# Kernel tuning notes

Hardware: AMD Instinct MI355X
Metric: run time of the kernel (lower is better)

Reference implementation:

```python
import jax, jax.numpy as jnp
import numpy as np

N = 500_000   # nodes
E = 1_250_000 # edges
CIN, H = 2, 64
EPS = 1e-5


def setup_inputs() -> dict:
    key = jax.random.key(0)
    ks = jax.random.split(key, 16)
    def w(k, i, o):
        return jax.random.normal(k, (i, o), jnp.float32) / np.sqrt(i)
    return {
        "x": jax.random.normal(ks[0], (N, CIN), jnp.float32),
        "edge_index": jax.random.randint(ks[1], (2, E), 0, N, jnp.int64),
        # SAGEConv layer 1 (lin_l on aggregated neighbors has bias, lin_r on root has none)
        "W1l": w(ks[2], CIN, H), "b1": jnp.zeros((H,), jnp.float32), "W1r": w(ks[3], CIN, H),
        "g1": jnp.ones((H,), jnp.float32), "be1": jnp.zeros((H,), jnp.float32),
        # SAGEConv layer 2
        "W2l": w(ks[4], H, H), "b2": jnp.zeros((H,), jnp.float32), "W2r": w(ks[5], H, H),
        "g2": jnp.ones((H,), jnp.float32), "be2": jnp.zeros((H,), jnp.float32),
        # SAGEConv layer 3 -> 1 channel
        "W3l": w(ks[6], H, 1), "b3": jnp.zeros((1,), jnp.float32), "W3r": w(ks[7], H, 1),
    }


def _sage(x, src, dst, Wl, b, Wr, n):
    # mean aggregation of source-node features into target nodes
    agg = jax.ops.segment_sum(x[src], dst, num_segments=n)           # [N, d_in]
    deg = jax.ops.segment_sum(jnp.ones((src.shape[0], 1), x.dtype), dst, num_segments=n)
    agg = agg / jnp.maximum(deg, 1.0)
    return agg @ Wl + b + x @ Wr


def _bn(x, g, be):
    m = jnp.mean(x, axis=0)
    v = jnp.var(x, axis=0)  # biased var, as torch BN uses for normalization
    return (x - m) * jax.lax.rsqrt(v + EPS) * g + be


def reference(x, edge_index, W1l, b1, W1r, g1, be1, W2l, b2, W2r, g2, be2, W3l, b3, W3r):
    src, dst = edge_index[0], edge_index[1]
    n = x.shape[0]
    x1 = jax.nn.relu(_bn(_sage(x, src, dst, W1l, b1, W1r, n), g1, be1))
    x2 = jax.nn.relu(_bn(_sage(x1, src, dst, W2l, b2, W2r, n), g2, be2))
    x2 = x2 + x1  # residual
    x3 = _sage(x2, src, dst, W3l, b3, W3r, n)
    return x3.reshape(-1)
```

## Files before the change

### kernel.cpp

```cpp
#include <hip/hip_runtime.h>

#define EPS 1e-5f

typedef __attribute__((ext_vector_type(8))) short bf16x8;
typedef __attribute__((ext_vector_type(4))) float f32x4;

__device__ __forceinline__ unsigned short f2bf(float f) {
    unsigned u = __float_as_uint(f);
    u += 0x7fffu + ((u >> 16) & 1u);
    return (unsigned short)(u >> 16);
}
__device__ __forceinline__ float bf2f(unsigned short s) {
    return __uint_as_float(((unsigned)s) << 16);
}

__global__ void k_detect(const int* __restrict__ ei, int* __restrict__ flag) {
    if (blockIdx.x == 0 && threadIdx.x == 0) {
        int is64 = 1;
        for (int k = 0; k < 16; ++k) is64 &= (ei[2 * k + 1] == 0) ? 1 : 0;
        *flag = is64;
    }
}

__global__ void k_hist(const int* __restrict__ ei, const int* __restrict__ flag,
                       int E, int* __restrict__ cnt) {
    int e = blockIdx.x * blockDim.x + threadIdx.x;
    if (e >= E) return;
    int d = (*flag) ? (int)((const long long*)ei)[E + e] : ei[E + e];
    atomicAdd(&cnt[d], 1);
}

__device__ __forceinline__ int block_incl_scan(int v, int tid, int* total) {
    __shared__ int wsum[4];
    __shared__ int tot;
#pragma unroll
    for (int o = 1; o < 64; o <<= 1) {
        int u = __shfl_up(v, o, 64);
        if ((tid & 63) >= o) v += u;
    }
    if ((tid & 63) == 63) wsum[tid >> 6] = v;
    __syncthreads();
    int w = tid >> 6, add = 0;
    if (w > 0) add += wsum[0];
    if (w > 1) add += wsum[1];
    if (w > 2) add += wsum[2];
    v += add;
    if (tid == 255) tot = v;
    __syncthreads();
    *total = tot;
    __syncthreads();
    return v;
}

__global__ __launch_bounds__(256) void k_scanA(const int* __restrict__ cnt, int n,
                                               int* __restrict__ bsums) {
    int tid = threadIdx.x;
    int idx = blockIdx.x * 1024 + tid * 4;
    int s = 0;
#pragma unroll
    for (int k = 0; k < 4; ++k) { int i = idx + k; if (i < n) s += cnt[i]; }
#pragma unroll
    for (int o = 32; o > 0; o >>= 1) s += __shfl_xor(s, o, 64);
    __shared__ int ws[4];
    if ((tid & 63) == 0) ws[tid >> 6] = s;
    __syncthreads();
    if (tid == 0) bsums[blockIdx.x] = ws[0] + ws[1] + ws[2] + ws[3];
}

__global__ __launch_bounds__(256) void k_scanB(int* __restrict__ bsums, int nb,
                                               int* __restrict__ rowptr, int N) {
    int tid = threadIdx.x;
    __shared__ int sh_carry;
    if (tid == 0) sh_carry = 0;
    __syncthreads();
    int niter = (nb + 255) / 256;
    for (int it = 0; it < niter; ++it) {
        int i = it * 256 + tid;
        int v = (i < nb) ? bsums[i] : 0;
        int tot;
        int inc = block_incl_scan(v, tid, &tot);
        int carry = sh_carry;
        if (i < nb) bsums[i] = carry + inc - v;
        __syncthreads();
        if (tid == 0) sh_carry = carry + tot;
        __syncthreads();
    }
    if (tid == 0) rowptr[N] = sh_carry;
}

__global__ __launch_bounds__(256) void k_scanC(int* __restrict__ cnt_rowptr, int n,
                                               const int* __restrict__ bsums,
                                               int* __restrict__ cursor) {
    int tid = threadIdx.x;
    int idx = blockIdx.x * 1024 + tid * 4;
    int v[4]; int s = 0;
#pragma unroll
    for (int k = 0; k < 4; ++k) { int i = idx + k; v[k] = (i < n) ? cnt_rowptr[i] : 0; s += v[k]; }
    int tot;
    int inc = block_incl_scan(s, tid, &tot);
    int off = bsums[blockIdx.x] + inc - s;
#pragma unroll
    for (int k = 0; k < 4; ++k) {
        int i = idx + k;
        if (i < n) { cnt_rowptr[i] = off; cursor[i] = off; off += v[k]; }
    }
}

__global__ void k_fill_range(const int* __restrict__ ei, const int* __restrict__ flag,
                             int E, int* __restrict__ cursor, int* __restrict__ csr,
                             int lo, int hi) {
    int e = blockIdx.x * blockDim.x + threadIdx.x;
    if (e >= E) return;
    int f = *flag;
    int d = f ? (int)((const long long*)ei)[E + e] : ei[E + e];
    if (d < lo || d >= hi) return;
    int s = f ? (int)((const long long*)ei)[e] : ei[e];
    int pos = atomicAdd(&cursor[d], 1);
    csr[pos] = s;
}

__global__ __launch_bounds__(256) void k_gather1m(
    const float* __restrict__ x, const int* __restrict__ rowptr,
    const int* __restrict__ csr, float* __restrict__ agg1,
    float* __restrict__ pmom, int n) {
    int tid = threadIdx.x;
    int i = blockIdx.x * 256 + tid;
    float m[14];
#pragma unroll
    for (int k = 0; k < 14; ++k) m[k] = 0.f;
    if (i < n) {
        int r0 = rowptr[i], r1 = rowptr[i + 1];
        float s0 = 0.f, s1 = 0.f;
        int j = r0;
        for (; j + 3 < r1; j += 4) {
            float2 v0 = ((const float2*)x)[csr[j]];
            float2 v1 = ((const float2*)x)[csr[j + 1]];
            float2 v2 = ((const float2*)x)[csr[j + 2]];
            float2 v3 = ((const float2*)x)[csr[j + 3]];
            s0 += v0.x + v1.x + v2.x + v3.x;
            s1 += v0.y + v1.y + v2.y + v3.y;
        }
        for (; j < r1; ++j) {
            float2 v = ((const float2*)x)[csr[j]];
            s0 += v.x; s1 += v.y;
        }
        float inv = 1.f / fmaxf((float)(r1 - r0), 1.f);
        float ax = s0 * inv, ay = s1 * inv;
        agg1[2 * i] = ax;
        agg1[2 * i + 1] = ay;
        float2 xv = ((const float2*)x)[i];
        m[0] = ax;        m[1] = ay;        m[2] = xv.x;      m[3] = xv.y;
        m[4] = ax * ax;   m[5] = ax * ay;   m[6] = ax * xv.x; m[7] = ax * xv.y;
        m[8] = ay * ay;   m[9] = ay * xv.x; m[10] = ay * xv.y;
        m[11] = xv.x * xv.x; m[12] = xv.x * xv.y; m[13] = xv.y * xv.y;
    }
#pragma unroll
    for (int k = 0; k < 14; ++k) {
#pragma unroll
        for (int o = 32; o > 0; o >>= 1) m[k] += __shfl_xor(m[k], o, 64);
    }
    __shared__ float red[4][14];
    int w = tid >> 6;
    if ((tid & 63) == 0) {
#pragma unroll
        for (int k = 0; k < 14; ++k) red[w][k] = m[k];
    }
    __syncthreads();
    if (tid < 14)
        pmom[(size_t)tid * gridDim.x + blockIdx.x] =
            red[0][tid] + red[1][tid] + red[2][tid] + red[3][tid];
}

__global__ __launch_bounds__(256) void k_bnfold1(
    const float* __restrict__ pmom, int gn,
    const float* __restrict__ W1l, const float* __restrict__ b1,
    const float* __restrict__ W1r,
    const float* __restrict__ g1, const float* __restrict__ be1,
    float* __restrict__ fold, float invN) {
    int tid = threadIdx.x;
    __shared__ float smom[14];
    __shared__ float ws[4];
    for (int k = 0; k < 14; ++k) {
        float s = 0.f;
        for (int idx = tid; idx < gn; idx += 256) s += pmom[(size_t)k * gn + idx];
#pragma unroll
        for (int o = 32; o > 0; o >>= 1) s += __shfl_xor(s, o, 64);
        if ((tid & 63) == 0) ws[tid >> 6] = s;
        __syncthreads();
        if (tid == 0) smom[k] = ws[0] + ws[1] + ws[2] + ws[3];
        __syncthreads();
    }
    if (tid < 64) {
        int c = tid;
        float w0 = W1l[c], w1 = W1l[64 + c], w2 = W1r[c], w3 = W1r[64 + c], w4 = b1[c];
        float lin = (smom[0] * w0 + smom[1] * w1 + smom[2] * w2 + smom[3] * w3) * invN;
        float mean = lin + w4;
        float q = smom[4] * w0 * w0 + smom[8] * w1 * w1 + smom[11] * w2 * w2 + smom[13] * w3 * w3
                + 2.f * (smom[5] * w0 * w1 + smom[6] * w0 * w2 + smom[7] * w0 * w3
                       + smom[9] * w1 * w2 + smom[10] * w1 * w3 + smom[12] * w2 * w3);
        float Eh2 = q * invN + 2.f * w4 * lin + w4 * w4;
        float var = Eh2 - mean * mean;
        float al = g1[c] * rsqrtf(var + EPS);
        float be = be1[c] - mean * al;
        fold[c]       = al * w0;
        fold[64 + c]  = al * w1;
        fold[128 + c] = al * w2;
        fold[192 + c] = al * w3;
        fold[256 + c] = al * w4 + be;
    }
}

__global__ __launch_bounds__(256) void k_sreduce(const float* __restrict__ pstats,
                                                 int nb, float* __restrict__ stats2) {
    int c = blockIdx.x, tid = threadIdx.x;
    float s = 0.f;
    for (int i = tid; i < nb; i += 256) s += pstats[(size_t)c * nb + i];
#pragma unroll
    for (int o = 32; o > 0; o >>= 1) s += __shfl_xor(s, o, 64);
    __shared__ float ws[4];
    if ((tid & 63) == 0) ws[tid >> 6] = s;
    __syncthreads();
    if (tid == 0) stats2[c] = ws[0] + ws[1] + ws[2] + ws[3];
}

__global__ void k_bnfin(const float* __restrict__ stats, const float* __restrict__ g,
                        const float* __restrict__ be, float* __restrict__ coef, float invN) {
    int c = threadIdx.x;
    float m = stats[c] * invN;
    float var = stats[64 + c] * invN - m * m;
    float a = g[c] * rsqrtf(var + EPS);
    coef[c] = a;
    coef[64 + c] = be[c] - m * a;
}

#define LROW 72

__global__ __launch_bounds__(256) void k_dense_pre(
    const float* __restrict__ agg1, const float* __restrict__ xin,
    const float* __restrict__ fold,
    const float* __restrict__ W2l, const float* __restrict__ b2,
    const float* __restrict__ W2r,
    const float* __restrict__ W3l, const float* __restrict__ W3r,
    unsigned short* __restrict__ y, unsigned short* __restrict__ z,
    float* __restrict__ t1, float* __restrict__ v1, int n) {
    __shared__ unsigned short lds_w[16 * 64 * 8];
    __shared__ __align__(16) unsigned short lds_y[4][16 * LROW];
    __shared__ __align__(16) unsigned short lds_z[4][16 * LROW];
    int tid = threadIdx.x, w = tid >> 6, l = tid & 63, ln = l & 15, kg = l >> 4;

    for (int idx = tid; idx < 4096; idx += 256) {
        int k = idx >> 6, c = idx & 63;
        int lane = ((k >> 3) & 3) * 16 + (c & 15);
        int fbase = ((k >> 5) * 4 + (c >> 4)) * 64 + lane;
        lds_w[fbase * 8 + (k & 7)] = f2bf(W2l[idx]);
        lds_w[(8 * 64 + fbase) * 8 + (k & 7)] = f2bf(W2r[idx]);
    }
    __syncthreads();

    float bb[4];
#pragma unroll
    for (int cs = 0; cs < 4; ++cs) bb[cs] = b2[cs * 16 + ln];

    float F0[16], F1[16], F2[16], F3[16], F4[16];
#pragma unroll
    for (int j = 0; j < 8; ++j) {
        int c = kg * 8 + j;
        F0[j] = fold[c];       F1[j] = fold[64 + c];  F2[j] = fold[128 + c];
        F3[j] = fold[192 + c]; F4[j] = fold[256 + c];
        c += 32;
        F0[8 + j] = fold[c];       F1[8 + j] = fold[64 + c];  F2[8 + j] = fold[128 + c];
        F3[8 + j] = fold[192 + c]; F4[8 + j] = fold[256 + c];
    }
    bf16x8 b3a, b3b;
#pragma unroll
    for (int j = 0; j < 8; ++j) {
        float va = (ln == 0) ? W3l[kg * 8 + j] : ((ln == 1) ? W3r[kg * 8 + j] : 0.f);
        float vb = (ln == 0) ? W3l[32 + kg * 8 + j] : ((ln == 1) ? W3r[32 + kg * 8 + j] : 0.f);
        b3a[j] = (short)f2bf(va);
        b3b[j] = (short)f2bf(vb);
    }

    unsigned short* Ys = lds_y[w];
    unsigned short* Zs = lds_z[w];
    const bf16x8* wfrag = (const bf16x8*)lds_w;
    int nt = (n + 15) >> 4;
    int stride = gridDim.x * 4;

#define LOADH(T, A)                                                          \
    {                                                                        \
        int row_ = ((T) << 4) + ln;                                          \
        int rr_ = (row_ < n) ? row_ : (n - 1);                               \
        A##a = ((const float2*)agg1)[rr_];                                   \
        A##x = ((const float2*)xin)[rr_];                                    \
    }

#define PROCESSH(T, A)                                                       \
    {                                                                        \
        bf16x8 u0_, u1_;                                                     \
        _Pragma("unroll")                                                    \
        for (int j = 0; j < 8; ++j) {                                        \
            float h0_ = fmaf(A##a.x, F0[j], fmaf(A##a.y, F1[j],              \
                        fmaf(A##x.x, F2[j], fmaf(A##x.y, F3[j], F4[j]))));   \
            float h1_ = fmaf(A##a.x, F0[8 + j], fmaf(A##a.y, F1[8 + j],      \
                        fmaf(A##x.x, F2[8 + j], fmaf(A##x.y, F3[8 + j], F4[8 + j])))); \
            u0_[j] = (short)f2bf(fmaxf(0.f, h0_));                           \
            u1_[j] = (short)f2bf(fmaxf(0.f, h1_));                           \
        }                                                                    \
        f32x4 ya_[4], za_[4], a3_;                                           \
        _Pragma("unroll")                                                    \
        for (int cs = 0; cs < 4; ++cs) {                                     \
            ya_[cs] = (f32x4){0.f, 0.f, 0.f, 0.f};                           \
            za_[cs] = (f32x4){0.f, 0.f, 0.f, 0.f};                           \
        }                                                                    \
        a3_ = (f32x4){0.f, 0.f, 0.f, 0.f};                                   \
        _Pragma("unroll")                                                    \
        for (int cs = 0; cs < 4; ++cs) {                                     \
            ya_[cs] = __builtin_amdgcn_mfma_f32_16x16x32_bf16(u0_, wfrag[(0 * 4 + cs) * 64 + l], ya_[cs], 0, 0, 0);  \
            ya_[cs] = __builtin_amdgcn_mfma_f32_16x16x32_bf16(u1_, wfrag[(1 * 4 + cs) * 64 + l], ya_[cs], 0, 0, 0);  \
            za_[cs] = __builtin_amdgcn_mfma_f32_16x16x32_bf16(u0_, wfrag[(8 + cs) * 64 + l], za_[cs], 0, 0, 0);      \
            za_[cs] = __builtin_amdgcn_mfma_f32_16x16x32_bf16(u1_, wfrag[(12 + cs) * 64 + l], za_[cs], 0, 0, 0);     \
        }                                                                    \
        a3_ = __builtin_amdgcn_mfma_f32_16x16x32_bf16(u0_, b3a, a3_, 0, 0, 0); \
        a3_ = __builtin_amdgcn_mfma_f32_16x16x32_bf16(u1_, b3b, a3_, 0, 0, 0); \
        _Pragma("unroll")                                                    \
        for (int cs = 0; cs < 4; ++cs) {                                     \
            _Pragma("unroll")                                                \
            for (int r = 0; r < 4; ++r) {                                    \
                Ys[(kg * 4 + r) * LROW + cs * 16 + ln] = f2bf(ya_[cs][r]);   \
                Zs[(kg * 4 + r) * LROW + cs * 16 + ln] = f2bf(za_[cs][r] + bb[cs]); \
            }                                                                \
        }                                                                    \
        int base_ = (T) << 4;                                                \
        if (ln < 2) {                                                        \
            float* d3_ = (ln == 0) ? t1 : v1;                                \
            _Pragma("unroll")                                                \
            for (int r = 0; r < 4; ++r) {                                    \
                int row_ = base_ + kg * 4 + r;                               \
                if (row_ < n) d3_[row_] = a3_[r];                            \
            }                                                                \
        }                                                                    \
        asm volatile("s_waitcnt lgkmcnt(0)" ::: "memory");                   \
        int orow_ = l >> 2, oc_ = (l & 3) * 16;                              \
        if (base_ + orow_ < n) {                                             \
            const bf16x8* yp_ = (const bf16x8*)(Ys + orow_ * LROW + oc_);    \
            const bf16x8* zp_ = (const bf16x8*)(Zs + orow_ * LROW + oc_);    \
            bf16x8* yd_ = (bf16x8*)(y + (size_t)(base_ + orow_) * 64 + oc_); \
            bf16x8* zd_ = (bf16x8*)(z + (size_t)(base_ + orow_) * 64 + oc_); \
            yd_[0] = yp_[0]; yd_[1] = yp_[1];                                \
            zd_[0] = zp_[0]; zd_[1] = zp_[1];                                \
        }                                                                    \
        asm volatile("s_waitcnt lgkmcnt(0)" ::: "memory");                   \
    }

    float2 Pa, Px, Qa, Qx;
    int t = blockIdx.x * 4 + w;
    if (t < nt) {
        LOADH(t, P);
        while (t < nt) {
            int t1_ = t + stride;
            if (t1_ < nt) LOADH(t1_, Q);
            PROCESSH(t, P);
            int t2_ = t1_ + stride;
            if (t2_ < nt) LOADH(t2_, P);
            if (t1_ < nt) PROCESSH(t1_, Q);
            t = t2_;
        }
    }
#undef LOADH
#undef PROCESSH
}

__global__ __launch_bounds__(256) void k_gather2b(
    const unsigned short* __restrict__ y, const int* __restrict__ rowptr,
    const int* __restrict__ csr, unsigned short* zh2,
    float* __restrict__ pstats, int n) {
    int tid = threadIdx.x;
    int lg = tid & 7;
    int gid0 = blockIdx.x * 32 + (tid >> 3);
    int gstep = gridDim.x * 32;
    float ls[8] = {0.f, 0.f, 0.f, 0.f, 0.f, 0.f, 0.f, 0.f};
    float lq[8] = {0.f, 0.f, 0.f, 0.f, 0.f, 0.f, 0.f, 0.f};

    for (int i = gid0; i < n; i += gstep) {
        bf16x8 z8 = *(const bf16x8*)(zh2 + (size_t)i * 64 + lg * 8);
        int r0 = rowptr[i], r1 = rowptr[i + 1];
        float s[8] = {0.f, 0.f, 0.f, 0.f, 0.f, 0.f, 0.f, 0.f};
        int j = r0;
        for (; j + 1 < r1; j += 2) {
            int a = csr[j], b = csr[j + 1];
            bf16x8 va = *(const bf16x8*)(y + (size_t)a * 64 + lg * 8);
            bf16x8 vb = *(const bf16x8*)(y + (size_t)b * 64 + lg * 8);
#pragma unroll
            for (int k = 0; k < 8; ++k)
                s[k] += bf2f((unsigned short)va[k]) + bf2f((unsigned short)vb[k]);
        }
        if (j < r1) {
            bf16x8 va = *(const bf16x8*)(y + (size_t)csr[j] * 64 + lg * 8);
#pragma unroll
            for (int k = 0; k < 8; ++k) s[k] += bf2f((unsigned short)va[k]);
        }
        float inv = 1.f / fmaxf((float)(r1 - r0), 1.f);
        bf16x8 hb;
#pragma unroll
        for (int k = 0; k < 8; ++k) {
            float h = fmaf(s[k], inv, bf2f((unsigned short)z8[k]));
            unsigned short b = f2bf(h);
            hb[k] = (short)b;
            float hf = bf2f(b);
            ls[k] += hf; lq[k] += hf * hf;
        }
        *(bf16x8*)(zh2 + (size_t)i * 64 + lg * 8) = hb;
    }

#pragma unroll
    for (int k = 0; k < 8; ++k) {
        ls[k] += __shfl_xor(ls[k], 8, 64);
        ls[k] += __shfl_xor(ls[k], 16, 64);
        ls[k] += __shfl_xor(ls[k], 32, 64);
        lq[k] += __shfl_xor(lq[k], 8, 64);
        lq[k] += __shfl_xor(lq[k], 16, 64);
        lq[k] += __shfl_xor(lq[k], 32, 64);
    }
    __shared__ float red[2][4][64];
    int w = tid >> 6;
    if ((tid & 63) < 8) {
#pragma unroll
        for (int k = 0; k < 8; ++k) {
            red[0][w][lg * 8 + k] = ls[k];
            red[1][w][lg * 8 + k] = lq[k];
        }
    }
    __syncthreads();
    if (tid < 128) {
        int c = tid & 63;
        int half = tid >> 6;
        float v = red[half][0][c] + red[half][1][c] + red[half][2][c] + red[half][3][c];
        pstats[(size_t)tid * gridDim.x + blockIdx.x] = v;
    }
}

__global__ __launch_bounds__(256) void k_finalize(
    const unsigned short* __restrict__ h2b,
    const float* __restrict__ t1, const float* __restrict__ v1,
    const float* __restrict__ coef2,
    const float* __restrict__ W3l, const float* __restrict__ W3r,
    float* __restrict__ tb, float* __restrict__ vb, int n) {
    int tid = threadIdx.x, w = tid >> 6, l = tid & 63, ln = l & 15, kg = l >> 4;

    float c2a[16], c2b[16];
#pragma unroll
    for (int j = 0; j < 8; ++j) {
        c2a[j]     = coef2[kg * 8 + j];       c2b[j]     = coef2[64 + kg * 8 + j];
        c2a[8 + j] = coef2[32 + kg * 8 + j];  c2b[8 + j] = coef2[96 + kg * 8 + j];
    }
    bf16x8 b3a, b3b;
#pragma unroll
    for (int j = 0; j < 8; ++j) {
        float va = (ln == 0) ? W3l[kg * 8 + j] : ((ln == 1) ? W3r[kg * 8 + j] : 0.f);
        float vb = (ln == 0) ? W3l[32 + kg * 8 + j] : ((ln == 1) ? W3r[32 + kg * 8 + j] : 0.f);
        b3a[j] = (short)f2bf(va);
        b3b[j] = (short)f2bf(vb);
    }

    int t = blockIdx.x * 4 + w;
    int nt = (n + 15) >> 4;
    if (t >= nt) return;
    int i0 = t << 4;
    int row = i0 + ln;
    int rr = (row < n) ? row : (n - 1);
    const unsigned short* hr = h2b + (size_t)rr * 64 + kg * 8;
    bf16x8 r0 = *(const bf16x8*)hr;
    bf16x8 r1 = *(const bf16x8*)(hr + 32);
    bf16x8 u0, u1;
#pragma unroll
    for (int j = 0; j < 8; ++j) {
        float f0 = bf2f((unsigned short)r0[j]);
        float f1 = bf2f((unsigned short)r1[j]);
        u0[j] = (short)f2bf(fmaxf(0.f, fmaf(f0, c2a[j], c2b[j])));
        u1[j] = (short)f2bf(fmaxf(0.f, fmaf(f1, c2a[8 + j], c2b[8 + j])));
    }
    f32x4 acc = (f32x4){0.f, 0.f, 0.f, 0.f};
    acc = __builtin_amdgcn_mfma_f32_16x16x32_bf16(u0, b3a, acc, 0, 0, 0);
    acc = __builtin_amdgcn_mfma_f32_16x16x32_bf16(u1, b3b, acc, 0, 0, 0);
    if (ln < 2) {
        float* d = (ln == 0) ? tb : vb;
        const float* s1 = (ln == 0) ? t1 : v1;
#pragma unroll
        for (int r = 0; r < 4; ++r) {
            int orow = i0 + kg * 4 + r;
            if (orow < n) d[orow] = acc[r] + s1[orow];
        }
    }
}

__global__ void k_gather3(const float* __restrict__ tb, const float* __restrict__ vb,
                          const int* __restrict__ rowptr, const int* __restrict__ csr,
                          const float* __restrict__ b3, float* __restrict__ out, int n) {
    int i = blockIdx.x * blockDim.x + threadIdx.x;
    if (i >= n) return;
    int r0 = rowptr[i], r1 = rowptr[i + 1];
    float s = 0.f;
    int j = r0;
    for (; j + 3 < r1; j += 4)
        s += tb[csr[j]] + tb[csr[j + 1]] + tb[csr[j + 2]] + tb[csr[j + 3]];
    for (; j < r1; ++j) s += tb[csr[j]];
    float inv = 1.f / fmaxf((float)(r1 - r0), 1.f);
    out[i] = fmaf(s, inv, b3[0] + vb[i]);
}

extern "C" void kernel_launch(void* const* d_in, const int* in_sizes, int n_in,
                              void* d_out, int out_size, void* d_ws, size_t ws_size,
                              hipStream_t stream) {
    const float* x   = (const float*)d_in[0];
    const int*   ei  = (const int*)d_in[1];
    const float* W1l = (const float*)d_in[2];
    const float* b1  = (const float*)d_in[3];
    const float* W1r = (const float*)d_in[4];
    const float* g1  = (const float*)d_in[5];
    const float* be1 = (const float*)d_in[6];
    const float* W2l = (const float*)d_in[7];
    const float* b2  = (const float*)d_in[8];
    const float* W2r = (const float*)d_in[9];
    const float* g2  = (const float*)d_in[10];
    const float* be2 = (const float*)d_in[11];
    const float* W3l = (const float*)d_in[12];
    const float* b3  = (const float*)d_in[13];
    const float* W3r = (const float*)d_in[14];

    int N = in_sizes[0] / 2;
    int E = in_sizes[1] / 2;

    float* ws   = (float*)d_ws;
    size_t nn   = (size_t)N;
    unsigned short* y   = (unsigned short*)ws;
    unsigned short* zh2 = (unsigned short*)(ws + 32 * nn);
    float* R     = ws + 64 * nn;
    int*   cursor = (int*)R;
    float* agg1   = R;
    float* tb     = R;
    float* vb     = R + nn;
    float* t1     = ws + 66 * nn;
    float* v1     = ws + 67 * nn;
    int*   rowptr = (int*)(ws + 68 * nn);
    int*   csr    = rowptr + (N + 1);
    int*   bsums  = csr + E;
    float* pstats = (float*)(bsums + 2048);
    float* pmom   = pstats + 128 * 2048;
    float* stats2 = pmom + 14 * 2048;
    float* coef2  = stats2 + 128;
    float* fold   = coef2 + 128;
    int*   flag   = (int*)(fold + 320);

    hipMemsetAsync(rowptr, 0, (size_t)(N + 1) * sizeof(int), stream);

    k_detect<<<1, 1, 0, stream>>>(ei, flag);

    int ge = (E + 255) / 256;
    int gn = (N + 255) / 256;
    int nb = (N + 1023) / 1024;
    k_hist<<<ge, 256, 0, stream>>>(ei, flag, E, rowptr);
    k_scanA<<<nb, 256, 0, stream>>>(rowptr, N, bsums);
    k_scanB<<<1, 256, 0, stream>>>(bsums, nb, rowptr, N);
    k_scanC<<<nb, 256, 0, stream>>>(rowptr, N, bsums, cursor);
    {
        const int NPASS = 4;
        int span = (N + NPASS - 1) / NPASS;
        for (int p = 0; p < NPASS; ++p) {
            int lo = p * span;
            int hi = min(N, lo + span);
            k_fill_range<<<ge, 256, 0, stream>>>(ei, flag, E, cursor, csr, lo, hi);
        }
    }

    k_gather1m<<<gn, 256, 0, stream>>>(x, rowptr, csr, agg1, pmom, N);
    k_bnfold1<<<1, 256, 0, stream>>>(pmom, gn, W1l, b1, W1r, g1, be1, fold,
                                     1.0f / (float)N);

    k_dense_pre<<<2048, 256, 0, stream>>>(agg1, x, fold, W2l, b2, W2r, W3l, W3r,
                                          y, zh2, t1, v1, N);

    k_gather2b<<<2048, 256, 0, stream>>>(y, rowptr, csr, zh2, pstats, N);
    k_sreduce<<<128, 256, 0, stream>>>(pstats, 2048, stats2);
    k_bnfin<<<1, 64, 0, stream>>>(stats2, g2, be2, coef2, 1.0f / (float)N);

    int nt = (N + 15) / 16;
    k_finalize<<<(nt + 3) / 4, 256, 0, stream>>>(zh2, t1, v1, coef2,
                                                 W3l, W3r, tb, vb, N);
    k_gather3<<<gn, 256, 0, stream>>>(tb, vb, rowptr, csr, b3, (float*)d_out, N);
}
```

Before: 361.0 us.

## Store MFMA outputs directly in permuted column layout and fuse BN stat reduction

The dense pre-kernel now writes y and z rows straight from MFMA accumulators as ushort4 stores in a permuted channel order, dropping the LDS staging buffers and their waits. Downstream consumers are adjusted for the permutation: the W3 weights in finalize and the BN gamma/beta lookup are reindexed. The separate stat-reduce and BN-finalize kernels are merged into one launch. This trades wide coalesced 16-byte stores for narrower 8-byte scattered stores and relies on every consumer of y/z handling the new channel order consistently.

```diff
diff --git a/kernel.cpp b/kernel.cpp
--- a/kernel.cpp
+++ b/kernel.cpp
@@ -13,6 +13,7 @@
 __device__ __forceinline__ float bf2f(unsigned short s) {
     return __uint_as_float(((unsigned)s) << 16);
 }
+
 
 __global__ void k_detect(const int* __restrict__ ei, int* __restrict__ flag) {
     if (blockIdx.x == 0 && threadIdx.x == 0) {
@@ -210,30 +211,35 @@
     }
 }
 
-__global__ __launch_bounds__(256) void k_sreduce(const float* __restrict__ pstats,
-                                                 int nb, float* __restrict__ stats2) {
+__global__ __launch_bounds__(256) void k_sredfin(
+    const float* __restrict__ pstats, int nb,
+    const float* __restrict__ g, const float* __restrict__ be,
+    float* __restrict__ coef, float invN) {
     int c = blockIdx.x, tid = threadIdx.x;
-    float s = 0.f;
-    for (int i = tid; i < nb; i += 256) s += pstats[(size_t)c * nb + i];
-#pragma unroll
-    for (int o = 32; o > 0; o >>= 1) s += __shfl_xor(s, o, 64);
-    __shared__ float ws[4];
-    if ((tid & 63) == 0) ws[tid >> 6] = s;
-    __syncthreads();
-    if (tid == 0) stats2[c] = ws[0] + ws[1] + ws[2] + ws[3];
-}
-
-__global__ void k_bnfin(const float* __restrict__ stats, const float* __restrict__ g,
-                        const float* __restrict__ be, float* __restrict__ coef, float invN) {
-    int c = threadIdx.x;
-    float m = stats[c] * invN;
-    float var = stats[64 + c] * invN - m * m;
-    float a = g[c] * rsqrtf(var + EPS);
-    coef[c] = a;
-    coef[64 + c] = be[c] - m * a;
-}
-
-#define LROW 72
+    float s = 0.f, q = 0.f;
+    for (int i = tid; i < nb; i += 256) {
+        s += pstats[(size_t)c * nb + i];
+        q += pstats[(size_t)(64 + c) * nb + i];
+    }
+#pragma unroll
+    for (int o = 32; o > 0; o >>= 1) {
+        s += __shfl_xor(s, o, 64);
+        q += __shfl_xor(q, o, 64);
+    }
+    __shared__ float ws[4], wq[4];
+    if ((tid & 63) == 0) { ws[tid >> 6] = s; wq[tid >> 6] = q; }
+    __syncthreads();
+    if (tid == 0) {
+        float S = ws[0] + ws[1] + ws[2] + ws[3];
+        float Q = wq[0] + wq[1] + wq[2] + wq[3];
+        float m = S * invN;
+        float var = Q * invN - m * m;
+        int o = (c & 3) * 16 + (c >> 2);
+        float a = g[o] * rsqrtf(var + EPS);
+        coef[c] = a;
+        coef[64 + c] = be[o] - m * a;
+    }
+}
 
 __global__ __launch_bounds__(256) void k_dense_pre(
     const float* __restrict__ agg1, const float* __restrict__ xin,
@@ -244,8 +250,6 @@
     unsigned short* __restrict__ y, unsigned short* __restrict__ z,
     float* __restrict__ t1, float* __restrict__ v1, int n) {
     __shared__ unsigned short lds_w[16 * 64 * 8];
-    __shared__ __align__(16) unsigned short lds_y[4][16 * LROW];
-    __shared__ __align__(16) unsigned short lds_z[4][16 * LROW];
     int tid = threadIdx.x, w = tid >> 6, l = tid & 63, ln = l & 15, kg = l >> 4;
 
     for (int idx = tid; idx < 4096; idx += 256) {
@@ -280,8 +284,6 @@
         b3b[j] = (short)f2bf(vb);
     }
 
-    unsigned short* Ys = lds_y[w];
-    unsigned short* Zs = lds_z[w];
     const bf16x8* wfrag = (const bf16x8*)lds_w;
     int nt = (n + 15) >> 4;
     int stride = gridDim.x * 4;
@@ -322,15 +324,20 @@
         }                                                                    \
         a3_ = __builtin_amdgcn_mfma_f32_16x16x32_bf16(u0_, b3a, a3_, 0, 0, 0); \
         a3_ = __builtin_amdgcn_mfma_f32_16x16x32_bf16(u1_, b3b, a3_, 0, 0, 0); \
+        int base_ = (T) << 4;                                                \
         _Pragma("unroll")                                                    \
-        for (int cs = 0; cs < 4; ++cs) {                                     \
-            _Pragma("unroll")                                                \
-            for (int r = 0; r < 4; ++r) {                                    \
-                Ys[(kg * 4 + r) * LROW + cs * 16 + ln] = f2bf(ya_[cs][r]);   \
-                Zs[(kg * 4 + r) * LROW + cs * 16 + ln] = f2bf(za_[cs][r] + bb[cs]); \
+        for (int r = 0; r < 4; ++r) {                                        \
+            int row_ = base_ + kg * 4 + r;                                   \
+            if (row_ < n) {                                                  \
+                ushort4 yv_, zv_;                                            \
+                yv_.x = f2bf(ya_[0][r]); yv_.y = f2bf(ya_[1][r]);            \
+                yv_.z = f2bf(ya_[2][r]); yv_.w = f2bf(ya_[3][r]);            \
+                zv_.x = f2bf(za_[0][r] + bb[0]); zv_.y = f2bf(za_[1][r] + bb[1]); \
+                zv_.z = f2bf(za_[2][r] + bb[2]); zv_.w = f2bf(za_[3][r] + bb[3]); \
+                *(ushort4*)(y + (size_t)row_ * 64 + ln * 4) = yv_;           \
+                *(ushort4*)(z + (size_t)row_ * 64 + ln * 4) = zv_;           \
             }                                                                \
         }                                                                    \
-        int base_ = (T) << 4;                                                \
         if (ln < 2) {                                                        \
             float* d3_ = (ln == 0) ? t1 : v1;                                \
             _Pragma("unroll")                                                \
@@ -339,17 +346,6 @@
                 if (row_ < n) d3_[row_] = a3_[r];                            \
             }                                                                \
         }                                                                    \
-        asm volatile("s_waitcnt lgkmcnt(0)" ::: "memory");                   \
-        int orow_ = l >> 2, oc_ = (l & 3) * 16;                              \
-        if (base_ + orow_ < n) {                                             \
-            const bf16x8* yp_ = (const bf16x8*)(Ys + orow_ * LROW + oc_);    \
-            const bf16x8* zp_ = (const bf16x8*)(Zs + orow_ * LROW + oc_);    \
-            bf16x8* yd_ = (bf16x8*)(y + (size_t)(base_ + orow_) * 64 + oc_); \
-            bf16x8* zd_ = (bf16x8*)(z + (size_t)(base_ + orow_) * 64 + oc_); \
-            yd_[0] = yp_[0]; yd_[1] = yp_[1];                                \
-            zd_[0] = zp_[0]; zd_[1] = zp_[1];                                \
-        }                                                                    \
-        asm volatile("s_waitcnt lgkmcnt(0)" ::: "memory");                   \
     }
 
     float2 Pa, Px, Qa, Qx;
@@ -456,8 +452,12 @@
     bf16x8 b3a, b3b;
 #pragma unroll
     for (int j = 0; j < 8; ++j) {
-        float va = (ln == 0) ? W3l[kg * 8 + j] : ((ln == 1) ? W3r[kg * 8 + j] : 0.f);
-        float vb = (ln == 0) ? W3l[32 + kg * 8 + j] : ((ln == 1) ? W3r[32 + kg * 8 + j] : 0.f);
+        int k0 = kg * 8 + j;
+        int k1 = 32 + kg * 8 + j;
+        int o0 = (k0 & 3) * 16 + (k0 >> 2);
+        int o1 = (k1 & 3) * 16 + (k1 >> 2);
+        float va = (ln == 0) ? W3l[o0] : ((ln == 1) ? W3r[o0] : 0.f);
+        float vb = (ln == 0) ? W3l[o1] : ((ln == 1) ? W3r[o1] : 0.f);
         b3a[j] = (short)f2bf(va);
         b3b[j] = (short)f2bf(vb);
     }
@@ -546,8 +546,7 @@
     int*   bsums  = csr + E;
     float* pstats = (float*)(bsums + 2048);
     float* pmom   = pstats + 128 * 2048;
-    float* stats2 = pmom + 14 * 2048;
-    float* coef2  = stats2 + 128;
+    float* coef2  = pmom + 14 * 2048;
     float* fold   = coef2 + 128;
     int*   flag   = (int*)(fold + 320);
 
@@ -580,8 +579,7 @@
                                           y, zh2, t1, v1, N);
 
     k_gather2b<<<2048, 256, 0, stream>>>(y, rowptr, csr, zh2, pstats, N);
-    k_sreduce<<<128, 256, 0, stream>>>(pstats, 2048, stats2);
-    k_bnfin<<<1, 64, 0, stream>>>(stats2, g2, be2, coef2, 1.0f / (float)N);
+    k_sredfin<<<64, 256, 0, stream>>>(pstats, 2048, g2, be2, coef2, 1.0f / (float)N);
 
     int nt = (N + 15) / 16;
     k_finalize<<<(nt + 3) / 4, 256, 0, stream>>>(zh2, t1, v1, coef2,
```

Result: faster. 350.3 us (-3.0%).
